# Kernel tuning notes

Hardware: AMD Instinct MI355X
Metric: run time of the kernel (lower is better)

Reference implementation:

```python
import jax, jax.numpy as jnp
import numpy as np

V, D, H, O = 50257, 256, 256, 10
L, N = 2048, 64


def setup_inputs() -> dict:
    key = jax.random.key(0)
    ks = jax.random.split(key, 20)
    s = 0.05
    p = {
        'x': jax.random.randint(ks[0], (L, N), 0, V, dtype=jnp.int64) if jax.config.jax_enable_x64 else jax.random.randint(ks[0], (L, N), 0, V, dtype=jnp.int32),
        'emb': jax.random.normal(ks[1], (V, D), jnp.float32) * s,
        'Wii': jax.random.normal(ks[2], (H, D), jnp.float32) * s, 'bii': jnp.zeros((H,), jnp.float32),
        'Whi': jax.random.normal(ks[3], (H, H), jnp.float32) * s, 'bhi': jnp.zeros((H,), jnp.float32),
        'Wif': jax.random.normal(ks[4], (H, D), jnp.float32) * s, 'bif': jnp.zeros((H,), jnp.float32),
        'Whf': jax.random.normal(ks[5], (H, H), jnp.float32) * s, 'bhf': jnp.zeros((H,), jnp.float32),
        'Wig': jax.random.normal(ks[6], (H, D), jnp.float32) * s, 'big': jnp.zeros((H,), jnp.float32),
        'Whg': jax.random.normal(ks[7], (H, H), jnp.float32) * s, 'bhg': jnp.zeros((H,), jnp.float32),
        'Wio': jax.random.normal(ks[8], (H, D), jnp.float32) * s, 'bio': jnp.zeros((H,), jnp.float32),
        'Who': jax.random.normal(ks[9], (H, H), jnp.float32) * s, 'bho': jnp.zeros((H,), jnp.float32),
        'Wout': jax.random.normal(ks[10], (O, H), jnp.float32) * s, 'bout': jnp.zeros((O,), jnp.float32),
    }
    return p


def _lstm_last_h(xe, Wii, bii, Whi, bhi, Wif, bif, Whf, bhf,
                 Wig, big, Whg, bhg, Wio, bio, Who, bho):
    # xe: [L, N, D]. Precompute all input-side gate projections in one big GEMM-like pass.
    xi = jnp.einsum('lnd,hd->lnh', xe, Wii) + bii
    xf = jnp.einsum('lnd,hd->lnh', xe, Wif) + bif
    xg = jnp.einsum('lnd,hd->lnh', xe, Wig) + big
    xo = jnp.einsum('lnd,hd->lnh', xe, Wio) + bio

    n = xe.shape[1]
    h0 = jnp.zeros((n, Whi.shape[0]), xe.dtype)
    c0 = jnp.zeros((n, Whi.shape[0]), xe.dtype)

    def step(carry, gates):
        h, c = carry
        gi, gf, gg, go = gates
        it = jax.nn.sigmoid(gi + h @ Whi.T + bhi)
        ft = jax.nn.sigmoid(gf + h @ Whf.T + bhf)
        gt = jnp.tanh(gg + h @ Whg.T + bhg)
        ot = jax.nn.sigmoid(go + h @ Who.T + bho)
        ct = ft * c + it * gt
        ht = ot * jnp.tanh(ct)
        return (ht, ct), None

    (hT, _), _ = jax.lax.scan(step, (h0, c0), (xi, xf, xg, xo))
    return hT  # [N, H]


def reference(x, emb, Wii, bii, Whi, bhi, Wif, bif, Whf, bhf,
              Wig, big, Whg, bhg, Wio, bio, Who, bho, Wout, bout):
    # EmbeddingBag with bag size 1 and mode='mean' == plain embedding lookup
    xe = emb[x]  # [L, N, D]
    hT = _lstm_last_h(xe, Wii, bii, Whi, bhi, Wif, bif, Whf, bhf,
                      Wig, big, Whg, bhg, Wio, bio, Who, bho)
    return hT @ Wout.T + bout  # [N, O]
```

## Files before the change

### kernel.cpp

```cpp
#include <hip/hip_runtime.h>


using half_t  = _Float16;
using half2_t = __attribute__((ext_vector_type(2))) _Float16;
using half8_t = __attribute__((ext_vector_type(8))) _Float16;
using f32x4   = __attribute__((ext_vector_type(4))) float;

#define L_SEQ   2048
#define CHUNK_L 1024
#define NB      64
#define DIM     256
#define P4      1024
#define CM      (CHUNK_L * NB)

#define OFF_GATES 0ull
#define SZ_GATES  ((unsigned long long)CM * P4 * 2)
#define OFF_EMBH  (OFF_GATES + SZ_GATES)
#define SZ_EMBH   (50257ull * 256 * 2)
#define OFF_WX    (OFF_EMBH + SZ_EMBH)
#define SZ_WX     (1024ull * 256 * 2)
#define OFF_WH    (OFF_WX + SZ_WX)
#define SZ_WH     (1024ull * 256 * 2)
#define OFF_B4    (OFF_WH + SZ_WH)
#define SZ_B4     (1024ull * 4)
#define OFF_ST    (OFF_B4 + SZ_B4)
#define SZ_ST     (2ull * NB * DIM * 4)
#define WS_NEED   (OFF_ST + SZ_ST)

__device__ __forceinline__ float sigm(float x) {
  x = fminf(fmaxf(x, -30.f), 30.f);
  return 1.f / (1.f + __expf(-x));
}
__device__ __forceinline__ float tanh_(float x) {
  x = fminf(fmaxf(x, -15.f), 15.f);
  float t = __expf(2.f * x);
  return (t - 1.f) / (t + 1.f);
}
__device__ __forceinline__ float dot8(half8_t w, half8_t h, float acc) {
  acc = __builtin_amdgcn_fdot2((half2_t)__builtin_shufflevector(w, w, 0, 1),
                               (half2_t)__builtin_shufflevector(h, h, 0, 1), acc, false);
  acc = __builtin_amdgcn_fdot2((half2_t)__builtin_shufflevector(w, w, 2, 3),
                               (half2_t)__builtin_shufflevector(h, h, 2, 3), acc, false);
  acc = __builtin_amdgcn_fdot2((half2_t)__builtin_shufflevector(w, w, 4, 5),
                               (half2_t)__builtin_shufflevector(h, h, 4, 5), acc, false);
  acc = __builtin_amdgcn_fdot2((half2_t)__builtin_shufflevector(w, w, 6, 7),
                               (half2_t)__builtin_shufflevector(h, h, 6, 7), acc, false);
  return acc;
}

__global__ void ws_too_small_kernel(float* out, float sz) {
  if (threadIdx.x == 0 && blockIdx.x == 0) out[0] = sz;
}

__global__ void cvt_emb_kernel(const float* __restrict__ src, half_t* __restrict__ dst,
                               int total8) {
  int i = blockIdx.x * blockDim.x + threadIdx.x;
  if (i >= total8) return;
  const float4* s = (const float4*)src + (size_t)i * 2;
  float4 a = s[0], b = s[1];
  half8_t o;
  o[0] = (half_t)a.x; o[1] = (half_t)a.y; o[2] = (half_t)a.z; o[3] = (half_t)a.w;
  o[4] = (half_t)b.x; o[5] = (half_t)b.y; o[6] = (half_t)b.z; o[7] = (half_t)b.w;
  *((half8_t*)dst + i) = o;
}

__global__ void pack_w_kernel(const float* __restrict__ Wii, const float* __restrict__ Whi,
                              const float* __restrict__ Wif, const float* __restrict__ Whf,
                              const float* __restrict__ Wig, const float* __restrict__ Whg,
                              const float* __restrict__ Wio, const float* __restrict__ Who,
                              const float* __restrict__ bii, const float* __restrict__ bhi,
                              const float* __restrict__ bif, const float* __restrict__ bhf,
                              const float* __restrict__ big_, const float* __restrict__ bhg,
                              const float* __restrict__ bio, const float* __restrict__ bho,
                              half_t* __restrict__ Wx4h, half_t* __restrict__ Wh4c,
                              float* __restrict__ b4) {
  int p = blockIdx.x;
  int k = threadIdx.x;
  int g = p >> 8, h = p & 255;
  const float* Wx = g == 0 ? Wii : g == 1 ? Wif : g == 2 ? Wig : Wio;
  const float* Wh = g == 0 ? Whi : g == 1 ? Whf : g == 2 ? Whg : Who;
  Wx4h[(size_t)p * DIM + k] = (half_t)Wx[h * DIM + k];
  Wh4c[((size_t)(k >> 3) * P4 + p) * 8 + (k & 7)] = (half_t)Wh[h * DIM + k];
  if (k == 0) {
    const float* bx = g == 0 ? bii : g == 1 ? bif : g == 2 ? big_ : bio;
    const float* bh = g == 0 ? bhi : g == 1 ? bhf : g == 2 ? bhg : bho;
    b4[p] = bx[h] + bh[h];
  }
}

#define BK   32
#define LSTR 40
__global__ __launch_bounds__(256) void gemm_gates_kernel(
    const half_t* __restrict__ embh, const int* __restrict__ xc,
    const half_t* __restrict__ Wx4h, const float* __restrict__ b4,
    half_t* __restrict__ gates) {
  __shared__ __align__(16) half_t As[128 * LSTR];
  __shared__ __align__(16) half_t Ws[128 * LSTR];
  const int tid  = threadIdx.x;
  const int lane = tid & 63;
  const int wave = tid >> 6;
  const int wm = wave >> 1, wn = wave & 1;
  const int M0 = blockIdx.x * 128;
  const int P0 = blockIdx.y * 128;
  const int r0 = tid >> 2, s0 = tid & 3;

  const size_t arow0 = (size_t)xc[M0 + r0] * DIM;
  const size_t arow1 = (size_t)xc[M0 + 64 + r0] * DIM;
  const size_t wrow0 = (size_t)(P0 + r0) * DIM;
  const size_t wrow1 = (size_t)(P0 + 64 + r0) * DIM;

  f32x4 acc[4][4] = {};
  const int fr = lane & 15;
  const int kq = lane >> 4;

  for (int kt = 0; kt < 8; ++kt) {
    const int k0 = kt * BK;
    half8_t a0 = *(const half8_t*)(embh + arow0 + k0 + s0 * 8);
    half8_t a1 = *(const half8_t*)(embh + arow1 + k0 + s0 * 8);
    half8_t w0 = *(const half8_t*)(Wx4h + wrow0 + k0 + s0 * 8);
    half8_t w1 = *(const half8_t*)(Wx4h + wrow1 + k0 + s0 * 8);
    __syncthreads();
    *(half8_t*)(As + r0 * LSTR + s0 * 8)        = a0;
    *(half8_t*)(As + (r0 + 64) * LSTR + s0 * 8) = a1;
    *(half8_t*)(Ws + r0 * LSTR + s0 * 8)        = w0;
    *(half8_t*)(Ws + (r0 + 64) * LSTR + s0 * 8) = w1;
    __syncthreads();
    half8_t af[4], bf[4];
#pragma unroll
    for (int mi = 0; mi < 4; ++mi)
      af[mi] = *(const half8_t*)(As + (wm * 64 + mi * 16 + fr) * LSTR + kq * 8);
#pragma unroll
    for (int ni = 0; ni < 4; ++ni)
      bf[ni] = *(const half8_t*)(Ws + (wn * 64 + ni * 16 + fr) * LSTR + kq * 8);
#pragma unroll
    for (int mi = 0; mi < 4; ++mi)
#pragma unroll
      for (int ni = 0; ni < 4; ++ni)
        acc[mi][ni] = __builtin_amdgcn_mfma_f32_16x16x32_f16(af[mi], bf[ni], acc[mi][ni], 0, 0, 0);
  }
  const int rbase = (lane >> 4) * 4;
#pragma unroll
  for (int ni = 0; ni < 4; ++ni) {
    const int p = P0 + wn * 64 + ni * 16 + fr;
    const float bias = b4[p];
#pragma unroll
    for (int mi = 0; mi < 4; ++mi) {
      const int m = M0 + wm * 64 + mi * 16 + rbase;
#pragma unroll
      for (int r = 0; r < 4; ++r)
        gates[(size_t)(m + r) * P4 + p] = (half_t)(acc[mi][ni][r] + bias);
    }
  }
}

__global__ __launch_bounds__(512, 2) void lstm_kernel(
    const half_t* __restrict__ gates, const half_t* __restrict__ Wh4c,
    const float* __restrict__ Wout, const float* __restrict__ bout,
    float* __restrict__ out, float* __restrict__ state,
    int first, int last) {
  const int n   = blockIdx.x;
  const int tid = threadIdx.x;
  const int j   = tid & 255;
  const int kh  = tid >> 8;
  __shared__ __align__(16) half_t wlds[8][P4][8];
  __shared__ half_t hbuf[2][DIM];
  __shared__ float  partial[4][DIM];
  __shared__ float  hfin[DIM];

  const half8_t* W8 = (const half8_t*)Wh4c;
  for (int i = tid; i < 8192; i += 512) {
    const int slot = i >> 10, p = i & 1023;
    const int kc = (slot >> 2) * 16 + 8 + (slot & 3);
    *(half8_t*)wlds[slot][p] = W8[kc * P4 + p];
  }
  const int kc0 = kh * 16;
  const int b0 = j, b1 = 256 + j, b2 = 512 + j, b3 = 768 + j;
  half8_t wreg[8][4];
#pragma unroll
  for (int kc = 0; kc < 8; ++kc) {
    wreg[kc][0] = W8[(kc0 + kc) * P4 + b0];
    wreg[kc][1] = W8[(kc0 + kc) * P4 + b1];
    wreg[kc][2] = W8[(kc0 + kc) * P4 + b2];
    wreg[kc][3] = W8[(kc0 + kc) * P4 + b3];
  }

  float c = 0.f, hkeep = 0.f;
  if (kh == 0) {
    float h0 = 0.f;
    if (!first) { h0 = state[n * DIM + j]; c = state[NB * DIM + n * DIM + j]; }
    hbuf[0][j] = (half_t)h0;
    hbuf[1][j] = (half_t)0.f;
    hkeep = h0;
  }
  __syncthreads();

  const half_t* gbase = gates + (size_t)n * P4;
  half_t g0 = (half_t)0.f, g1 = g0, g2 = g0, g3 = g0;
  if (kh == 0) { g0 = gbase[b0]; g1 = gbase[b1]; g2 = gbase[b2]; g3 = gbase[b3]; }

#pragma unroll 1
  for (int l = 0; l < CHUNK_L; ++l) {
    float a0 = 0.f, a1 = 0.f, a2 = 0.f, a3 = 0.f;
    if (kh == 0) { a0 = (float)g0; a1 = (float)g1; a2 = (float)g2; a3 = (float)g3; }
    const half8_t* hp = (const half8_t*)hbuf[l & 1] + kc0;
#pragma unroll
    for (int kc = 0; kc < 8; ++kc) {
      const half8_t h8 = hp[kc];
      a0 = dot8(wreg[kc][0], h8, a0);
      a1 = dot8(wreg[kc][1], h8, a1);
      a2 = dot8(wreg[kc][2], h8, a2);
      a3 = dot8(wreg[kc][3], h8, a3);
    }
#pragma unroll
    for (int s = 0; s < 4; ++s) {
      const half8_t h8 = hp[8 + s];
      const int slot = kh * 4 + s;
      a0 = dot8(*(const half8_t*)wlds[slot][b0], h8, a0);
      a1 = dot8(*(const half8_t*)wlds[slot][b1], h8, a1);
      a2 = dot8(*(const half8_t*)wlds[slot][b2], h8, a2);
      a3 = dot8(*(const half8_t*)wlds[slot][b3], h8, a3);
    }
#pragma unroll
    for (int s = 0; s < 4; ++s) {
      const half8_t h8 = hp[12 + s];
      const half8_t* wp = W8 + (size_t)(kc0 + 12 + s) * P4;
      a0 = dot8(wp[b0], h8, a0);
      a1 = dot8(wp[b1], h8, a1);
      a2 = dot8(wp[b2], h8, a2);
      a3 = dot8(wp[b3], h8, a3);
    }
    if (kh == 0) {
      const half_t* gp2 = gbase + (size_t)(l + 1) * NB * P4;
      g0 = gp2[b0]; g1 = gp2[b1]; g2 = gp2[b2]; g3 = gp2[b3];
    } else {
      partial[0][j] = a0; partial[1][j] = a1; partial[2][j] = a2; partial[3][j] = a3;
    }
    __syncthreads();
    if (kh == 0) {
      a0 += partial[0][j]; a1 += partial[1][j]; a2 += partial[2][j]; a3 += partial[3][j];
      const float it = sigm(a0), ft = sigm(a1), gt = tanh_(a2), ot = sigm(a3);
      c = ft * c + it * gt;
      const float h = ot * tanh_(c);
      hbuf[(l + 1) & 1][j] = (half_t)h;
      hkeep = h;
    }
    __syncthreads();
  }
  if (kh == 0) {
    if (!last) { state[n * DIM + j] = hkeep; state[NB * DIM + n * DIM + j] = c; }
    hfin[j] = hkeep;
  }
  __syncthreads();
  if (last && tid < 10) {
    float s = bout[tid];
    const float* wrow = Wout + tid * DIM;
#pragma unroll 4
    for (int k = 0; k < DIM; ++k) s += hfin[k] * wrow[k];
    out[n * 10 + tid] = s;
  }
}

extern "C" void kernel_launch(void* const* d_in, const int* in_sizes, int n_in,
                              void* d_out, int out_size, void* d_ws, size_t ws_size,
                              hipStream_t stream) {
  const int*   x    = (const int*)d_in[0];
  const float* emb  = (const float*)d_in[1];
  const float* Wii  = (const float*)d_in[2];  const float* bii = (const float*)d_in[3];
  const float* Whi  = (const float*)d_in[4];  const float* bhi = (const float*)d_in[5];
  const float* Wif  = (const float*)d_in[6];  const float* bif = (const float*)d_in[7];
  const float* Whf  = (const float*)d_in[8];  const float* bhf = (const float*)d_in[9];
  const float* Wig  = (const float*)d_in[10]; const float* big_ = (const float*)d_in[11];
  const float* Whg  = (const float*)d_in[12]; const float* bhg = (const float*)d_in[13];
  const float* Wio  = (const float*)d_in[14]; const float* bio = (const float*)d_in[15];
  const float* Who  = (const float*)d_in[16]; const float* bho = (const float*)d_in[17];
  const float* Wout = (const float*)d_in[18]; const float* bout = (const float*)d_in[19];
  float* out = (float*)d_out;

  if (ws_size < WS_NEED) {
    hipLaunchKernelGGL(ws_too_small_kernel, dim3(1), dim3(64), 0, stream, out, (float)ws_size);
    return;
  }
  char* ws = (char*)d_ws;
  half_t* gates = (half_t*)(ws + OFF_GATES);
  half_t* embh  = (half_t*)(ws + OFF_EMBH);
  half_t* Wx4h  = (half_t*)(ws + OFF_WX);
  half_t* Wh4c  = (half_t*)(ws + OFF_WH);
  float*  b4    = (float*)(ws + OFF_B4);
  float*  state = (float*)(ws + OFF_ST);

  const int total8 = 50257 * 32;
  hipLaunchKernelGGL(cvt_emb_kernel, dim3((total8 + 255) / 256), dim3(256), 0, stream,
                     emb, embh, total8);
  hipLaunchKernelGGL(pack_w_kernel, dim3(1024), dim3(256), 0, stream,
                     Wii, Whi, Wif, Whf, Wig, Whg, Wio, Who,
                     bii, bhi, bif, bhf, big_, bhg, bio, bho,
                     Wx4h, Wh4c, b4);
  hipLaunchKernelGGL(gemm_gates_kernel, dim3(CM / 128, P4 / 128), dim3(256), 0, stream,
                     embh, x, Wx4h, b4, gates);
  hipLaunchKernelGGL(lstm_kernel, dim3(NB), dim3(512), 0, stream,
                     gates, Wh4c, Wout, bout, out, state, 1, 0);
  hipLaunchKernelGGL(gemm_gates_kernel, dim3(CM / 128, P4 / 128), dim3(256), 0, stream,
                     embh, x + (size_t)CHUNK_L * NB, Wx4h, b4, gates);
  hipLaunchKernelGGL(lstm_kernel, dim3(NB), dim3(512), 0, stream,
                     gates, Wh4c, Wout, bout, out, state, 0, 1);
}
```

Before: 3.374 ms.

## Keep recurrent weights in registers and LDS, move gate prefetch to second half-block

The LSTM recurrence kernel now holds 12 of each thread's 16 weight chunks in registers instead of 8, with the remaining 4 in LDS. This removes the per-step global loads of weights entirely. Gate-input loading and prefetch move from the kh==0 half to the kh==1 half, with the next-step load issued at the top of the loop so it overlaps the dot products. The partial sums are exchanged through a single float4 LDS write and read. Higher register pressure (48 half8 vectors, pinned with empty asm) risks spills or lower occupancy under the 512x2 launch bounds.

After: 3.241 ms. 3.9% less time.

```diff
diff --git a/kernel.cpp b/kernel.cpp
--- a/kernel.cpp
+++ b/kernel.cpp
@@ -163,48 +163,59 @@
   const int j   = tid & 255;
   const int kh  = tid >> 8;
   __shared__ __align__(16) half_t wlds[8][P4][8];
-  __shared__ half_t hbuf[2][DIM];
-  __shared__ float  partial[4][DIM];
-  __shared__ float  hfin[DIM];
+  __shared__ __align__(16) half_t hbuf[2][DIM];
+  __shared__ __align__(16) float  partial4[DIM][4];
+  __shared__ float hfin[DIM];
 
   const half8_t* W8 = (const half8_t*)Wh4c;
   for (int i = tid; i < 8192; i += 512) {
     const int slot = i >> 10, p = i & 1023;
-    const int kc = (slot >> 2) * 16 + 8 + (slot & 3);
+    const int kc = (slot >> 2) * 16 + 12 + (slot & 3);
     *(half8_t*)wlds[slot][p] = W8[kc * P4 + p];
   }
   const int kc0 = kh * 16;
   const int b0 = j, b1 = 256 + j, b2 = 512 + j, b3 = 768 + j;
-  half8_t wreg[8][4];
-#pragma unroll
-  for (int kc = 0; kc < 8; ++kc) {
+  half8_t wreg[12][4];
+#pragma unroll
+  for (int kc = 0; kc < 12; ++kc) {
     wreg[kc][0] = W8[(kc0 + kc) * P4 + b0];
     wreg[kc][1] = W8[(kc0 + kc) * P4 + b1];
     wreg[kc][2] = W8[(kc0 + kc) * P4 + b2];
     wreg[kc][3] = W8[(kc0 + kc) * P4 + b3];
   }
+#pragma unroll
+  for (int kc = 0; kc < 12; ++kc)
+#pragma unroll
+    for (int g = 0; g < 4; ++g)
+      asm volatile("" : "+v"(wreg[kc][g]));
 
   float c = 0.f, hkeep = 0.f;
   if (kh == 0) {
     float h0 = 0.f;
     if (!first) { h0 = state[n * DIM + j]; c = state[NB * DIM + n * DIM + j]; }
     hbuf[0][j] = (half_t)h0;
-    hbuf[1][j] = (half_t)0.f;
     hkeep = h0;
   }
+  const half_t* gbase = gates + (size_t)n * P4;
+  float g0 = 0.f, g1 = 0.f, g2 = 0.f, g3 = 0.f;
+  if (kh == 1) {
+    g0 = (float)gbase[b0]; g1 = (float)gbase[b1];
+    g2 = (float)gbase[b2]; g3 = (float)gbase[b3];
+  }
   __syncthreads();
-
-  const half_t* gbase = gates + (size_t)n * P4;
-  half_t g0 = (half_t)0.f, g1 = g0, g2 = g0, g3 = g0;
-  if (kh == 0) { g0 = gbase[b0]; g1 = gbase[b1]; g2 = gbase[b2]; g3 = gbase[b3]; }
 
 #pragma unroll 1
   for (int l = 0; l < CHUNK_L; ++l) {
     float a0 = 0.f, a1 = 0.f, a2 = 0.f, a3 = 0.f;
-    if (kh == 0) { a0 = (float)g0; a1 = (float)g1; a2 = (float)g2; a3 = (float)g3; }
+    half_t ng0, ng1, ng2, ng3;
+    if (kh == 1) {
+      a0 = g0; a1 = g1; a2 = g2; a3 = g3;
+      const half_t* gp2 = gbase + (size_t)(l + 1) * NB * P4;
+      ng0 = gp2[b0]; ng1 = gp2[b1]; ng2 = gp2[b2]; ng3 = gp2[b3];
+    }
     const half8_t* hp = (const half8_t*)hbuf[l & 1] + kc0;
 #pragma unroll
-    for (int kc = 0; kc < 8; ++kc) {
+    for (int kc = 0; kc < 12; ++kc) {
       const half8_t h8 = hp[kc];
       a0 = dot8(wreg[kc][0], h8, a0);
       a1 = dot8(wreg[kc][1], h8, a1);
@@ -213,31 +224,22 @@
     }
 #pragma unroll
     for (int s = 0; s < 4; ++s) {
-      const half8_t h8 = hp[8 + s];
+      const half8_t h8 = hp[12 + s];
       const int slot = kh * 4 + s;
       a0 = dot8(*(const half8_t*)wlds[slot][b0], h8, a0);
       a1 = dot8(*(const half8_t*)wlds[slot][b1], h8, a1);
       a2 = dot8(*(const half8_t*)wlds[slot][b2], h8, a2);
       a3 = dot8(*(const half8_t*)wlds[slot][b3], h8, a3);
     }
-#pragma unroll
-    for (int s = 0; s < 4; ++s) {
-      const half8_t h8 = hp[12 + s];
-      const half8_t* wp = W8 + (size_t)(kc0 + 12 + s) * P4;
-      a0 = dot8(wp[b0], h8, a0);
-      a1 = dot8(wp[b1], h8, a1);
-      a2 = dot8(wp[b2], h8, a2);
-      a3 = dot8(wp[b3], h8, a3);
-    }
-    if (kh == 0) {
-      const half_t* gp2 = gbase + (size_t)(l + 1) * NB * P4;
-      g0 = gp2[b0]; g1 = gp2[b1]; g2 = gp2[b2]; g3 = gp2[b3];
-    } else {
-      partial[0][j] = a0; partial[1][j] = a1; partial[2][j] = a2; partial[3][j] = a3;
+    if (kh == 1) {
+      float4 pv; pv.x = a0; pv.y = a1; pv.z = a2; pv.w = a3;
+      *(float4*)partial4[j] = pv;
+      g0 = (float)ng0; g1 = (float)ng1; g2 = (float)ng2; g3 = (float)ng3;
     }
     __syncthreads();
     if (kh == 0) {
-      a0 += partial[0][j]; a1 += partial[1][j]; a2 += partial[2][j]; a3 += partial[3][j];
+      float4 pv = *(const float4*)partial4[j];
+      a0 += pv.x; a1 += pv.y; a2 += pv.z; a3 += pv.w;
       const float it = sigm(a0), ft = sigm(a1), gt = tanh_(a2), ot = sigm(a3);
       c = ft * c + it * gt;
       const float h = ot * tanh_(c);
```

## Split LSTM recurrence across four blocks per sequence with global h exchange

Applied to the files above, without the earlier changes.

The recurrent LSTM kernel now uses four blocks per batch element instead of one, each owning 64 hidden units across all four gates. Each block's slice of the recurrent weights is held entirely in registers, which removes the LDS and global weight reads from the inner loop. Every timestep, the blocks exchange the new hidden state through tagged 64-bit words in global memory, spinning with atomics until the tag matches. This trades per-step cross-block synchronisation latency for lower per-block compute and register-resident weights. It relies on all 256 blocks being resident at once, or the spin-waits can deadlock.

Measured after the change: 3.626 ms. 1.07x slower.

```diff
diff --git a/kernel.cpp b/kernel.cpp
--- a/kernel.cpp
+++ b/kernel.cpp
@@ -25,7 +25,9 @@
 #define SZ_B4     (1024ull * 4)
 #define OFF_ST    (OFF_B4 + SZ_B4)
 #define SZ_ST     (2ull * NB * DIM * 4)
-#define WS_NEED   (OFF_ST + SZ_ST)
+#define OFF_HX    (OFF_ST + SZ_ST)
+#define SZ_HX     ((unsigned long long)NB * 2 * 128 * 8)
+#define WS_NEED   (OFF_HX + SZ_HX)
 
 __device__ __forceinline__ float sigm(float x) {
   x = fminf(fmaxf(x, -30.f), 30.f);
@@ -47,6 +49,12 @@
                                (half2_t)__builtin_shufflevector(h, h, 6, 7), acc, false);
   return acc;
 }
+__device__ __forceinline__ half_t us2h(unsigned short x) {
+  return __builtin_bit_cast(half_t, x);
+}
+__device__ __forceinline__ unsigned short h2us(half_t x) {
+  return __builtin_bit_cast(unsigned short, x);
+}
 
 __global__ void ws_too_small_kernel(float* out, float sz) {
   if (threadIdx.x == 0 && blockIdx.x == 0) out[0] = sz;
@@ -73,9 +81,11 @@
                               const float* __restrict__ big_, const float* __restrict__ bhg,
                               const float* __restrict__ bio, const float* __restrict__ bho,
                               half_t* __restrict__ Wx4h, half_t* __restrict__ Wh4c,
-                              float* __restrict__ b4) {
+                              float* __restrict__ b4, unsigned long long* __restrict__ hx) {
   int p = blockIdx.x;
   int k = threadIdx.x;
+  int idx = p * 256 + k;
+  if (idx < NB * 2 * 128) hx[idx] = 0ull;
   int g = p >> 8, h = p & 255;
   const float* Wx = g == 0 ? Wii : g == 1 ? Wif : g == 2 ? Wig : Wio;
   const float* Wh = g == 0 ? Whi : g == 1 ? Whf : g == 2 ? Whg : Who;
@@ -153,109 +163,111 @@
   }
 }
 
-__global__ __launch_bounds__(512, 2) void lstm_kernel(
-    const half_t* __restrict__ gates, const half_t* __restrict__ Wh4c,
-    const float* __restrict__ Wout, const float* __restrict__ bout,
-    float* __restrict__ out, float* __restrict__ state,
-    int first, int last) {
-  const int n   = blockIdx.x;
+#define DW(i)  half8_t W##i = Wp8[((kh << 4) + i) * P4 + p];
+#define PIN4(a,b,c,d) asm volatile("" : "+v"(a), "+v"(b), "+v"(c), "+v"(d));
+#define DOT(i) a = dot8(W##i, hp[i], a);
+
+__global__ __launch_bounds__(512, 2)
+void lstm4_kernel(const half_t* __restrict__ gates, const half_t* __restrict__ Wh4c,
+                  const float* __restrict__ Wout, const float* __restrict__ bout,
+                  float* __restrict__ out, float* __restrict__ state,
+                  unsigned long long* __restrict__ hx,
+                  int base, int first, int last) {
+  const int b   = blockIdx.x;
+  const int q   = (b >> 3) & 3;
+  const int n   = (b & 7) | ((b >> 5) << 3);
   const int tid = threadIdx.x;
-  const int j   = tid & 255;
+  const int o   = tid & 255;
   const int kh  = tid >> 8;
-  __shared__ __align__(16) half_t wlds[8][P4][8];
+  const int g   = o >> 6, ul = o & 63;
+  const int u   = (q << 6) | ul;
+  const int p   = (g << 8) | u;
+
   __shared__ half_t hbuf[2][DIM];
-  __shared__ float  partial[4][DIM];
-  __shared__ float  hfin[DIM];
-
-  const half8_t* W8 = (const half8_t*)Wh4c;
-  for (int i = tid; i < 8192; i += 512) {
-    const int slot = i >> 10, p = i & 1023;
-    const int kc = (slot >> 2) * 16 + 8 + (slot & 3);
-    *(half8_t*)wlds[slot][p] = W8[kc * P4 + p];
-  }
-  const int kc0 = kh * 16;
-  const int b0 = j, b1 = 256 + j, b2 = 512 + j, b3 = 768 + j;
-  half8_t wreg[8][4];
-#pragma unroll
-  for (int kc = 0; kc < 8; ++kc) {
-    wreg[kc][0] = W8[(kc0 + kc) * P4 + b0];
-    wreg[kc][1] = W8[(kc0 + kc) * P4 + b1];
-    wreg[kc][2] = W8[(kc0 + kc) * P4 + b2];
-    wreg[kc][3] = W8[(kc0 + kc) * P4 + b3];
-  }
-
-  float c = 0.f, hkeep = 0.f;
-  if (kh == 0) {
-    float h0 = 0.f;
-    if (!first) { h0 = state[n * DIM + j]; c = state[NB * DIM + n * DIM + j]; }
-    hbuf[0][j] = (half_t)h0;
-    hbuf[1][j] = (half_t)0.f;
-    hkeep = h0;
-  }
+  __shared__ float  pl[256][2];
+  __shared__ float  glds[256];
+
+  const half8_t* Wp8 = (const half8_t*)Wh4c;
+  DW(0) DW(1) DW(2) DW(3) DW(4) DW(5) DW(6) DW(7)
+  DW(8) DW(9) DW(10) DW(11) DW(12) DW(13) DW(14) DW(15)
+  PIN4(W0, W1, W2, W3) PIN4(W4, W5, W6, W7)
+  PIN4(W8, W9, W10, W11) PIN4(W12, W13, W14, W15)
+
+  const int  isP = ((tid >> 5) == (8 + q));
+  const int  t0  = tid & 31;
+  const int  u0  = (q << 6) + 2 * t0;
+  unsigned long long* hxn = hx + n * 256;
+
+  float c0 = 0.f, c1 = 0.f;
+  if (tid < 256) hbuf[0][tid] = first ? (half_t)0.f : (half_t)state[n * DIM + tid];
+  if (isP && !first) {
+    c0 = state[NB * DIM + n * DIM + u0];
+    c1 = state[NB * DIM + n * DIM + u0 + 1];
+  }
+  const half_t* gch = gates + (size_t)n * P4 + p;
+  float gprev = 0.f;
+  if (tid < 256) gprev = (float)gch[0];
   __syncthreads();
 
-  const half_t* gbase = gates + (size_t)n * P4;
-  half_t g0 = (half_t)0.f, g1 = g0, g2 = g0, g3 = g0;
-  if (kh == 0) { g0 = gbase[b0]; g1 = gbase[b1]; g2 = gbase[b2]; g3 = gbase[b3]; }
-
+  int par = 0;
 #pragma unroll 1
   for (int l = 0; l < CHUNK_L; ++l) {
-    float a0 = 0.f, a1 = 0.f, a2 = 0.f, a3 = 0.f;
-    if (kh == 0) { a0 = (float)g0; a1 = (float)g1; a2 = (float)g2; a3 = (float)g3; }
-    const half8_t* hp = (const half8_t*)hbuf[l & 1] + kc0;
-#pragma unroll
-    for (int kc = 0; kc < 8; ++kc) {
-      const half8_t h8 = hp[kc];
-      a0 = dot8(wreg[kc][0], h8, a0);
-      a1 = dot8(wreg[kc][1], h8, a1);
-      a2 = dot8(wreg[kc][2], h8, a2);
-      a3 = dot8(wreg[kc][3], h8, a3);
-    }
-#pragma unroll
-    for (int s = 0; s < 4; ++s) {
-      const half8_t h8 = hp[8 + s];
-      const int slot = kh * 4 + s;
-      a0 = dot8(*(const half8_t*)wlds[slot][b0], h8, a0);
-      a1 = dot8(*(const half8_t*)wlds[slot][b1], h8, a1);
-      a2 = dot8(*(const half8_t*)wlds[slot][b2], h8, a2);
-      a3 = dot8(*(const half8_t*)wlds[slot][b3], h8, a3);
-    }
-#pragma unroll
-    for (int s = 0; s < 4; ++s) {
-      const half8_t h8 = hp[12 + s];
-      const half8_t* wp = W8 + (size_t)(kc0 + 12 + s) * P4;
-      a0 = dot8(wp[b0], h8, a0);
-      a1 = dot8(wp[b1], h8, a1);
-      a2 = dot8(wp[b2], h8, a2);
-      a3 = dot8(wp[b3], h8, a3);
-    }
-    if (kh == 0) {
-      const half_t* gp2 = gbase + (size_t)(l + 1) * NB * P4;
-      g0 = gp2[b0]; g1 = gp2[b1]; g2 = gp2[b2]; g3 = gp2[b3];
-    } else {
-      partial[0][j] = a0; partial[1][j] = a1; partial[2][j] = a2; partial[3][j] = a3;
-    }
+    float gnext = 0.f;
+    if (tid < 256) {
+      glds[o] = gprev;
+      gnext = (float)gch[(size_t)(l + 1) * NB * P4];
+    }
+    const half8_t* hp = (const half8_t*)hbuf[par] + (kh << 4);
+    float a = 0.f;
+    DOT(0) DOT(1) DOT(2) DOT(3) DOT(4) DOT(5) DOT(6) DOT(7)
+    DOT(8) DOT(9) DOT(10) DOT(11) DOT(12) DOT(13) DOT(14) DOT(15)
+    pl[o][kh] = a;
     __syncthreads();
-    if (kh == 0) {
-      a0 += partial[0][j]; a1 += partial[1][j]; a2 += partial[2][j]; a3 += partial[3][j];
-      const float it = sigm(a0), ft = sigm(a1), gt = tanh_(a2), ot = sigm(a3);
-      c = ft * c + it * gt;
-      const float h = ot * tanh_(c);
-      hbuf[(l + 1) & 1][j] = (half_t)h;
-      hkeep = h;
-    }
+
+    const unsigned long long tag = (unsigned long long)(base + l + 1);
+    unsigned long long* slot = hxn + ((par ^ 1) << 7);
+    if (isP) {
+      float hh[2];
+#pragma unroll
+      for (int j = 0; j < 2; ++j) {
+        const int lu = 2 * t0 + j;
+        const float ai  = pl[lu][0]       + pl[lu][1]       + glds[lu];
+        const float af_ = pl[64 + lu][0]  + pl[64 + lu][1]  + glds[64 + lu];
+        const float ag  = pl[128 + lu][0] + pl[128 + lu][1] + glds[128 + lu];
+        const float ao  = pl[192 + lu][0] + pl[192 + lu][1] + glds[192 + lu];
+        float& cc = (j == 0) ? c0 : c1;
+        cc = sigm(af_) * cc + sigm(ai) * tanh_(ag);
+        hh[j] = sigm(ao) * tanh_(cc);
+      }
+      const unsigned long long qw =
+          (tag << 32) |
+          ((unsigned long long)h2us((half_t)hh[1]) << 16) |
+          (unsigned long long)h2us((half_t)hh[0]);
+      atomicExch(&slot[(q << 5) + t0], qw);
+    }
+    if (tid < 128) {
+      unsigned long long v;
+      while (((v = atomicAdd(&slot[tid], 0ull)) >> 32) != tag)
+        __builtin_amdgcn_s_sleep(1);
+      hbuf[par ^ 1][2 * tid]     = us2h((unsigned short)(v & 0xffff));
+      hbuf[par ^ 1][2 * tid + 1] = us2h((unsigned short)((v >> 16) & 0xffff));
+    }
+    gprev = gnext;
+    par ^= 1;
     __syncthreads();
   }
-  if (kh == 0) {
-    if (!last) { state[n * DIM + j] = hkeep; state[NB * DIM + n * DIM + j] = c; }
-    hfin[j] = hkeep;
-  }
-  __syncthreads();
-  if (last && tid < 10) {
+  if (!last) {
+    if (q == 0 && tid < 256) state[n * DIM + tid] = (float)hbuf[0][tid];
+    if (isP) {
+      state[NB * DIM + n * DIM + u0]     = c0;
+      state[NB * DIM + n * DIM + u0 + 1] = c1;
+    }
+  }
+  if (last && q == 0 && tid < 10) {
     float s = bout[tid];
     const float* wrow = Wout + tid * DIM;
 #pragma unroll 4
-    for (int k = 0; k < DIM; ++k) s += hfin[k] * wrow[k];
+    for (int k = 0; k < DIM; ++k) s += (float)hbuf[0][k] * wrow[k];
     out[n * 10 + tid] = s;
   }
 }
@@ -287,6 +299,7 @@
   half_t* Wh4c  = (half_t*)(ws + OFF_WH);
   float*  b4    = (float*)(ws + OFF_B4);
   float*  state = (float*)(ws + OFF_ST);
+  unsigned long long* hx = (unsigned long long*)(ws + OFF_HX);
 
   const int total8 = 50257 * 32;
   hipLaunchKernelGGL(cvt_emb_kernel, dim3((total8 + 255) / 256), dim3(256), 0, stream,
@@ -294,13 +307,13 @@
   hipLaunchKernelGGL(pack_w_kernel, dim3(1024), dim3(256), 0, stream,
                      Wii, Whi, Wif, Whf, Wig, Whg, Wio, Who,
                      bii, bhi, bif, bhf, big_, bhg, bio, bho,
-                     Wx4h, Wh4c, b4);
+                     Wx4h, Wh4c, b4, hx);
   hipLaunchKernelGGL(gemm_gates_kernel, dim3(CM / 128, P4 / 128), dim3(256), 0, stream,
                      embh, x, Wx4h, b4, gates);
-  hipLaunchKernelGGL(lstm_kernel, dim3(NB), dim3(512), 0, stream,
-                     gates, Wh4c, Wout, bout, out, state, 1, 0);
+  hipLaunchKernelGGL(lstm4_kernel, dim3(256), dim3(512), 0, stream,
+                     gates, Wh4c, Wout, bout, out, state, hx, 0, 1, 0);
   hipLaunchKernelGGL(gemm_gates_kernel, dim3(CM / 128, P4 / 128), dim3(256), 0, stream,
                      embh, x + (size_t)CHUNK_L * NB, Wx4h, b4, gates);
-  hipLaunchKernelGGL(lstm_kernel, dim3(NB), dim3(512), 0, stream,
-                     gates, Wh4c, Wout, bout, out, state, 0, 1);
-}
+  hipLaunchKernelGGL(lstm4_kernel, dim3(256), dim3(512), 0, stream,
+                     gates, Wh4c, Wout, bout, out, state, hx, CHUNK_L, 0, 1);
+}
```
